# Performance work log

Hardware: AMD Instinct MI355X
Metric: run time of the kernel (lower is better)

The kernel has to match this reference:

```python
import jax, jax.numpy as jnp
import numpy as np

DMODEL = 1024
NHEAD = 16
DHEAD = DMODEL // NHEAD

def _layernorm(x, g, b, eps=1e-5):
    mu = jnp.mean(x, axis=-1, keepdims=True)
    var = jnp.var(x, axis=-1, keepdims=True)
    return (x - mu) * jax.lax.rsqrt(var + eps) * g + b

def setup_inputs() -> dict:
    key = jax.random.key(0)
    ks = jax.random.split(key, 12)
    b, lq, lv, d = 2, 2048, 2048, DMODEL
    s = 1.0 / np.sqrt(d)
    return {
        "q": jax.random.normal(ks[0], (b, lq, d), jnp.float32),
        "k": jax.random.normal(ks[1], (b, lv, d), jnp.float32),
        "v": jax.random.normal(ks[2], (b, lv, d), jnp.float32),
        "qln_g": jnp.ones((d,), jnp.float32),
        "qln_b": jnp.zeros((d,), jnp.float32),
        "kvln_g": jnp.ones((d,), jnp.float32),
        "kvln_b": jnp.zeros((d,), jnp.float32),
        "Wq": jax.random.normal(ks[3], (d, d), jnp.float32) * s,
        "Wk": jax.random.normal(ks[4], (d, d), jnp.float32) * s,
        "Wv": jax.random.normal(ks[5], (d, d), jnp.float32) * s,
        "Wg": jax.random.normal(ks[6], (d, d), jnp.float32) * s,
        "bg": jnp.zeros((d,), jnp.float32),
        "Wo": jax.random.normal(ks[7], (d, d), jnp.float32) * s,
    }

def reference(q, k, v, qln_g, qln_b, kvln_g, kvln_b, Wq, Wk, Wv, Wg, bg, Wo):
    b, lq, d = q.shape
    lv = v.shape[1]
    qn = _layernorm(q, qln_g, qln_b)           # [b, lq, d]
    q_ = qn @ Wq.T
    kk = _layernorm(k, kvln_g, kvln_b) @ Wk.T
    vv = _layernorm(v, kvln_g, kvln_b) @ Wv.T
    qh = q_.reshape(b, lq, NHEAD, DHEAD)       # bqhd
    kh = kk.reshape(b, lv, NHEAD, DHEAD)
    vh = vv.reshape(b, lv, NHEAD, DHEAD)
    scores = jnp.einsum('bqhd,bkhd->bhqk', qh, kh) / np.sqrt(DHEAD)
    attn = jax.nn.softmax(scores, axis=-1)
    y = jnp.einsum('bhqk,bkhd->bqhd', attn, vh).reshape(b, lq, d)
    g = jax.nn.sigmoid(qn @ Wg.T + bg)
    return (y * g) @ Wo.T
```

## Files before the change

### kernel.cpp

```cpp
#include <hip/hip_runtime.h>
#include <hip/hip_bf16.h>

#define DMODEL 1024
#define NHEAD  16
#define DHEAD  64
#define BATCH  2
#define LQ     2048
#define LV     2048
#define ROWS   (BATCH*LQ)
#define WELEMS (DMODEL*DMODEL)
#define BH     (BATCH*NHEAD)

typedef short bf16x8 __attribute__((ext_vector_type(8)));
typedef float f32x4  __attribute__((ext_vector_type(4)));

__device__ __forceinline__ float bf2f(unsigned short s) {
    union { unsigned u; float f; } v; v.u = ((unsigned)s) << 16;
    return v.f;
}
__device__ __forceinline__ unsigned pk_bf(float a, float b) {
    union { __hip_bfloat162 h; unsigned u; } c;
    c.h = __float22bfloat162_rn(make_float2(a, b));
    return c.u;
}

__device__ __forceinline__ void cp16_g2l(const void* g, void* l) {
    __builtin_amdgcn_global_load_lds(
        (const __attribute__((address_space(1))) void*)g,
        (__attribute__((address_space(3))) void*)l,
        16, 0, 0);
}

#define QSCALE (0.125f * 1.4426950408889634f)

__global__ __launch_bounds__(256) void prep_kernel(
    const float* q, const float* k, const float* v,
    const float* qg, const float* qb, const float* kvg, const float* kvb,
    const float* Wq, const float* Wk, const float* Wv, const float* Wg, const float* Wo,
    unsigned short* qn, unsigned short* kn, unsigned short* vn, unsigned short* wb)
{
    __shared__ float rs[4], rq[4];
    int z = blockIdx.y;
    if (z < 5) {
        if (blockIdx.x >= WELEMS / 1024) return;
        const float* srcs[5] = {Wq, Wk, Wv, Wg, Wo};
        const float* s = srcs[z];
        unsigned short* d = wb + (size_t)z * WELEMS;
        int i = (blockIdx.x * 256 + threadIdx.x) * 4;
        float4 x = *(const float4*)(s + i);
        uint2 o = make_uint2(pk_bf(x.x, x.y), pk_bf(x.z, x.w));
        *(uint2*)(d + i) = o;
        return;
    }
    int row = blockIdx.x;
    const float *x, *gp, *bp; unsigned short* o;
    if      (z == 5) { x = q; gp = qg;  bp = qb;  o = qn; }
    else if (z == 6) { x = k; gp = kvg; bp = kvb; o = kn; }
    else             { x = v; gp = kvg; bp = kvb; o = vn; }

    int col = threadIdx.x * 4;
    float4 xv = *(const float4*)(x + (size_t)row * DMODEL + col);
    float s  = xv.x + xv.y + xv.z + xv.w;
    float sq = xv.x*xv.x + xv.y*xv.y + xv.z*xv.z + xv.w*xv.w;
    #pragma unroll
    for (int off = 1; off < 64; off <<= 1) { s += __shfl_xor(s, off); sq += __shfl_xor(sq, off); }

    int wave = threadIdx.x >> 6, lane = threadIdx.x & 63;
    if (lane == 0) { rs[wave] = s; rq[wave] = sq; }
    __syncthreads();
    float ts = rs[0] + rs[1] + rs[2] + rs[3];
    float tq = rq[0] + rq[1] + rq[2] + rq[3];
    float mu  = ts * (1.0f / DMODEL);
    float var = tq * (1.0f / DMODEL) - mu * mu;
    float inv = rsqrtf(var + 1e-5f);

    float4 gv = *(const float4*)(gp + col);
    float4 bv = *(const float4*)(bp + col);
    float r0 = (xv.x - mu) * inv * gv.x + bv.x;
    float r1 = (xv.y - mu) * inv * gv.y + bv.y;
    float r2 = (xv.z - mu) * inv * gv.z + bv.z;
    float r3 = (xv.w - mu) * inv * gv.w + bv.w;
    *(uint2*)(o + (size_t)row * DMODEL + col) = make_uint2(pk_bf(r0, r1), pk_bf(r2, r3));
}

template<int MODE>
__device__ __forceinline__ void gemm256_core(
    const unsigned short* A, const unsigned short* Bw,
    unsigned short* Obf, const float* bias, float scale,
    unsigned short* Al, unsigned short* Bl, int bm, int bn)
{
    int tid  = threadIdx.x;
    int w = tid >> 6, l = tid & 63, quad = l >> 4, L = l & 15;
    int wm = w >> 2, wn = w & 3;

    int c16 = (l & 7) ^ (l >> 3);
    const unsigned short* gAs = A  + (size_t)(bm * 256 + w * 32 + (l >> 3)) * DMODEL + c16 * 8;
    const unsigned short* gBs = Bw + (size_t)(bn * 256 + w * 32 + (l >> 3)) * DMODEL + c16 * 8;
    int dstE = w * 2048;

    #define STG_A(t) do { const unsigned short* s_ = gAs + (t) * 64;          \
        unsigned short* d_ = Al + (((t) & 1) * 16384) + dstE;                 \
        cp16_g2l(s_,              d_);                                        \
        cp16_g2l(s_ +  8 * DMODEL, d_ +  512);                                \
        cp16_g2l(s_ + 16 * DMODEL, d_ + 1024);                                \
        cp16_g2l(s_ + 24 * DMODEL, d_ + 1536); } while (0)
    #define STG_B(t) do { const unsigned short* s_ = gBs + (t) * 64;          \
        unsigned short* d_ = Bl + (((t) & 1) * 16384) + dstE;                 \
        cp16_g2l(s_,              d_);                                        \
        cp16_g2l(s_ +  8 * DMODEL, d_ +  512);                                \
        cp16_g2l(s_ + 16 * DMODEL, d_ + 1024);                                \
        cp16_g2l(s_ + 24 * DMODEL, d_ + 1536); } while (0)

    int sw = (L & 7) << 3;
    int o0 = ( 0 + quad * 8) ^ sw;
    int o1 = (32 + quad * 8) ^ sw;

    f32x4 acc[8][4];
    #pragma unroll
    for (int i = 0; i < 8; ++i)
        #pragma unroll
        for (int j = 0; j < 4; ++j) acc[i][j] = (f32x4){0.f, 0.f, 0.f, 0.f};

    STG_A(0); STG_B(0);

    const int NT = DMODEL / 64;
    for (int g = 0; g < NT; ++g) {
        int s = g & 1;
        if (g + 1 < NT) { STG_A(g + 1); STG_B(g + 1); }
        if (g + 1 < NT) asm volatile("s_waitcnt vmcnt(8)" ::: "memory");
        else            asm volatile("s_waitcnt vmcnt(0)" ::: "memory");
        __builtin_amdgcn_s_barrier();

        const unsigned short* Ab = Al + s * 16384 + (wm * 128) * 64;
        const unsigned short* Bb = Bl + s * 16384 + (wn * 64) * 64;
        bf16x8 bfr[4][2];
        #pragma unroll
        for (int j = 0; j < 4; ++j) {
            bfr[j][0] = *(const bf16x8*)&Bb[(j * 16 + L) * 64 + o0];
            bfr[j][1] = *(const bf16x8*)&Bb[(j * 16 + L) * 64 + o1];
        }
        __builtin_amdgcn_s_setprio(1);
        #pragma unroll
        for (int i2 = 0; i2 < 8; ++i2) {
            bf16x8 a0 = *(const bf16x8*)&Ab[(i2 * 16 + L) * 64 + o0];
            bf16x8 a1 = *(const bf16x8*)&Ab[(i2 * 16 + L) * 64 + o1];
            #pragma unroll
            for (int j = 0; j < 4; ++j) {
                if (MODE == 3) {
                    acc[i2][j] = __builtin_amdgcn_mfma_f32_16x16x32_bf16(a0, bfr[j][0], acc[i2][j], 0, 0, 0);
                    acc[i2][j] = __builtin_amdgcn_mfma_f32_16x16x32_bf16(a1, bfr[j][1], acc[i2][j], 0, 0, 0);
                } else {
                    acc[i2][j] = __builtin_amdgcn_mfma_f32_16x16x32_bf16(bfr[j][0], a0, acc[i2][j], 0, 0, 0);
                    acc[i2][j] = __builtin_amdgcn_mfma_f32_16x16x32_bf16(bfr[j][1], a1, acc[i2][j], 0, 0, 0);
                }
            }
        }
        __builtin_amdgcn_s_setprio(0);
        __builtin_amdgcn_s_barrier();
    }
    #undef STG_A
    #undef STG_B

    #pragma unroll
    for (int i = 0; i < 8; ++i) {
        #pragma unroll
        for (int j = 0; j < 4; ++j) {
            f32x4 a = acc[i][j];
            if (MODE == 3) {
                int gcol  = bn * 256 + wn * 64 + j * 16 + L;
                int grow0 = bm * 256 + wm * 128 + i * 16 + quad * 4;
                int b = grow0 >> 11, key0 = grow0 & 2047;
                int h = gcol >> 6,   dd   = gcol & 63;
                uint2 o = make_uint2(pk_bf(a[0], a[1]), pk_bf(a[2], a[3]));
                *(uint2*)&Obf[(((size_t)(b * NHEAD + h) * DHEAD + dd) << 11) + key0] = o;
            } else {
                int grow  = bm * 256 + wm * 128 + i * 16 + L;
                int gcol0 = bn * 256 + wn * 64 + j * 16 + quad * 4;
                size_t idx = (size_t)grow * DMODEL + gcol0;
                if (MODE == 0) {
                    uint2 o = make_uint2(pk_bf(a[0] * scale, a[1] * scale),
                                         pk_bf(a[2] * scale, a[3] * scale));
                    *(uint2*)&Obf[idx] = o;
                } else {
                    float4 bv = *(const float4*)&bias[gcol0];
                    float s0 = 1.0f / (1.0f + __expf(-(a[0] + bv.x)));
                    float s1 = 1.0f / (1.0f + __expf(-(a[1] + bv.y)));
                    float s2 = 1.0f / (1.0f + __expf(-(a[2] + bv.z)));
                    float s3 = 1.0f / (1.0f + __expf(-(a[3] + bv.w)));
                    *(uint2*)&Obf[idx] = make_uint2(pk_bf(s0, s1), pk_bf(s2, s3));
                }
            }
        }
    }
}

__global__ __launch_bounds__(512, 2) void gemm256_kernel(
    const unsigned short* qn, const unsigned short* kn, const unsigned short* vn,
    const unsigned short* wb,
    unsigned short* qs, unsigned short* kkp, unsigned short* vt, unsigned short* gate,
    const float* bg)
{
    __shared__ __align__(16) unsigned short Al[2 * 256 * 64];
    __shared__ __align__(16) unsigned short Bl[2 * 256 * 64];
    int f = blockIdx.x, xcd = f & 7, s = f >> 3;
    int z  = xcd & 3;
    int bm = ((xcd >> 2) << 3) | (s >> 2);
    int bn = s & 3;
    switch (z) {
        case 0:  gemm256_core<0>(qn, wb + 0 * WELEMS, qs,   nullptr, QSCALE, Al, Bl, bm, bn); break;
        case 1:  gemm256_core<0>(kn, wb + 1 * WELEMS, kkp,  nullptr, 1.0f,   Al, Bl, bm, bn); break;
        case 2:  gemm256_core<3>(vn, wb + 2 * WELEMS, vt,   nullptr, 1.0f,   Al, Bl, bm, bn); break;
        default: gemm256_core<1>(qn, wb + 3 * WELEMS, gate, bg,      1.0f,   Al, Bl, bm, bn); break;
    }
}

template<int MODE>
__device__ __forceinline__ void gemm_bt_core(
    const unsigned short* A, const unsigned short* Bw,
    unsigned short* Obf, float* Of32, const float* bias, float scale,
    unsigned short* Al, unsigned short* Bl, int bm, int bn)
{
    int tid  = threadIdx.x;
    int wave = tid >> 6, lane = tid & 63, quad = lane >> 4, L = lane & 15;
    int wm = wave >> 1, wn = wave & 1;

    int srow = wave * 16 + (lane >> 2);
    int scol = (lane & 3) * 8;
    const unsigned short* gA = A  + (size_t)(bm * 128 + srow) * DMODEL + scol;
    const unsigned short* gB = Bw + (size_t)(bn * 128 + srow) * DMODEL + scol;
    int lofs0 = wave * 16 * 32;
    int lofs1 = (64 + wave * 16) * 32;

    f32x4 acc[4][4];
    #pragma unroll
    for (int i = 0; i < 4; ++i)
        #pragma unroll
        for (int j = 0; j < 4; ++j) acc[i][j] = (f32x4){0.f, 0.f, 0.f, 0.f};

    cp16_g2l(gA,               Al + lofs0);
    cp16_g2l(gA + 64 * DMODEL, Al + lofs1);
    cp16_g2l(gB,               Bl + lofs0);
    cp16_g2l(gB + 64 * DMODEL, Bl + lofs1);

    int buf = 0;
    for (int k0 = 0; k0 < DMODEL; k0 += 32, buf ^= 1) {
        __syncthreads();
        if (k0 + 32 < DMODEL) {
            int nb = (buf ^ 1) * (128 * 32);
            cp16_g2l(gA + k0 + 32,               Al + nb + lofs0);
            cp16_g2l(gA + 64 * DMODEL + k0 + 32, Al + nb + lofs1);
            cp16_g2l(gB + k0 + 32,               Bl + nb + lofs0);
            cp16_g2l(gB + 64 * DMODEL + k0 + 32, Bl + nb + lofs1);
        }
        const unsigned short* Ab = Al + buf * (128 * 32);
        const unsigned short* Bb = Bl + buf * (128 * 32);
        bf16x8 af[4], bfr[4];
        #pragma unroll
        for (int i = 0; i < 4; ++i)
            af[i] = *(const bf16x8*)&Ab[(wm * 64 + i * 16 + L) * 32 + quad * 8];
        #pragma unroll
        for (int j = 0; j < 4; ++j)
            bfr[j] = *(const bf16x8*)&Bb[(wn * 64 + j * 16 + L) * 32 + quad * 8];
        #pragma unroll
        for (int i = 0; i < 4; ++i)
            #pragma unroll
            for (int j = 0; j < 4; ++j) {
                if (MODE == 3)
                    acc[i][j] = __builtin_amdgcn_mfma_f32_16x16x32_bf16(af[i], bfr[j], acc[i][j], 0, 0, 0);
                else
                    acc[i][j] = __builtin_amdgcn_mfma_f32_16x16x32_bf16(bfr[j], af[i], acc[i][j], 0, 0, 0);
            }
    }

    #pragma unroll
    for (int i = 0; i < 4; ++i) {
        #pragma unroll
        for (int j = 0; j < 4; ++j) {
            f32x4 a = acc[i][j];
            int grow  = bm * 128 + wm * 64 + i * 16 + L;
            int gcol0 = bn * 128 + wn * 64 + j * 16 + quad * 4;
            size_t idx = (size_t)grow * DMODEL + gcol0;
            if (MODE == 2) {
                *(f32x4*)&Of32[idx] = a;
            } else if (MODE == 0) {
                uint2 o = make_uint2(pk_bf(a[0] * scale, a[1] * scale),
                                     pk_bf(a[2] * scale, a[3] * scale));
                *(uint2*)&Obf[idx] = o;
            }
        }
    }
}

__device__ __forceinline__ void xcd_map(int& bm, int& bn) {
    int f = blockIdx.y * 8 + blockIdx.x;
    int xcd = f & 7, s = f >> 3;
    bn = s & 7;
    bm = ((s >> 3) << 3) | xcd;
}

__global__ __launch_bounds__(256) void gemm_f32out_kernel(
    const unsigned short* A, const unsigned short* Bw, float* O)
{
    __shared__ __align__(16) unsigned short Al[2 * 128 * 32];
    __shared__ __align__(16) unsigned short Bl[2 * 128 * 32];
    int bm, bn; xcd_map(bm, bn);
    gemm_bt_core<2>(A, Bw, nullptr, O, nullptr, 1.0f, Al, Bl, bm, bn);
}

__global__ __launch_bounds__(256, 4) void attn_kernel(
    const unsigned short* qs, const unsigned short* kk, const unsigned short* vt,
    const unsigned short* gate, unsigned short* yg)
{
    __shared__ __align__(16) unsigned short Kl[2 * 64 * 64];
    __shared__ __align__(16) unsigned short Vl[2 * 64 * 64];

    int tid  = threadIdx.x;
    int wave = tid >> 6, lane = tid & 63, quad = lane >> 4, L = lane & 15;

    int f  = blockIdx.y * 32 + blockIdx.x;
    int bh = (f & 7) * 4 + ((f >> 3) & 3);
    int qt = f >> 5;
    int bb = bh >> 4, h = bh & 15;
    int q0 = qt * 64;

    const unsigned short* Qb =
        qs + ((size_t)(bb * LQ + q0 + wave * 16 + L)) * DMODEL + h * DHEAD;
    bf16x8 aq0 = *(const bf16x8*)(Qb + quad * 8);
    bf16x8 aq1 = *(const bf16x8*)(Qb + 32 + quad * 8);

    f32x4 acc[4];
    #pragma unroll
    for (int nt = 0; nt < 4; ++nt) acc[nt] = (f32x4){0.f, 0.f, 0.f, 0.f};
    f32x4 lacc = (f32x4){0.f, 0.f, 0.f, 0.f};
    bf16x8 ones;
    #pragma unroll
    for (int j = 0; j < 8; ++j) ones[j] = (short)0x3F80;

    int rloc = lane >> 3;
    int c16  = (lane & 7) ^ rloc;
    int key0 = (wave & 1) * 32 + (rloc >> 2) * 8 + (wave >> 1) * 4 + (rloc & 3);

    const unsigned short* gK = kk + (size_t)bb * LV * DMODEL + h * DHEAD
                                  + (size_t)key0 * DMODEL + c16 * 8;
    const unsigned short* gV = vt + ((size_t)((bb * NHEAD + h) * DHEAD
                                  + wave * 16 + rloc)) * LV + c16 * 8;
    char* KlB = (char*)Kl;
    char* VlB = (char*)Vl;
    int dst0 = wave * 2048;

    cp16_g2l(gK,               KlB + dst0);
    cp16_g2l(gK + 16 * DMODEL, KlB + dst0 + 1024);
    cp16_g2l(gV,               VlB + dst0);
    cp16_g2l(gV + 8 * LV,      VlB + dst0 + 1024);

    int sl0 = (quad ^ (L & 7)) * 8;
    int buf = 0;
    for (int it = 0; it < LV / 64; ++it, buf ^= 1) {
        __syncthreads();
        if (it + 1 < LV / 64) {
            gK += 64 * DMODEL; gV += 64;
            int nb = (buf ^ 1) * 8192 + dst0;
            cp16_g2l(gK,               KlB + nb);
            cp16_g2l(gK + 16 * DMODEL, KlB + nb + 1024);
            cp16_g2l(gV,               VlB + nb);
            cp16_g2l(gV + 8 * LV,      VlB + nb + 1024);
        }
        const unsigned short* Kb = Kl + buf * 4096;
        const unsigned short* Vb = Vl + buf * 4096;

        f32x4 zz[4];
        __builtin_amdgcn_s_setprio(1);
        #pragma unroll
        for (int kt = 0; kt < 4; ++kt) {
            bf16x8 bk0 = *(const bf16x8*)&Kb[(kt * 16 + L) * 64 + sl0];
            bf16x8 bk1 = *(const bf16x8*)&Kb[(kt * 16 + L) * 64 + (sl0 ^ 32)];
            f32x4 z = (f32x4){0.f, 0.f, 0.f, 0.f};
            z = __builtin_amdgcn_mfma_f32_16x16x32_bf16(bk0, aq0, z, 0, 0, 0);
            z = __builtin_amdgcn_mfma_f32_16x16x32_bf16(bk1, aq1, z, 0, 0, 0);
            zz[kt] = z;
        }
        __builtin_amdgcn_s_setprio(0);

        union { unsigned u[4]; bf16x8 h; } pa0, pa1;
        pa0.u[0] = pk_bf(__builtin_amdgcn_exp2f(zz[0][0]), __builtin_amdgcn_exp2f(zz[0][1]));
        pa0.u[1] = pk_bf(__builtin_amdgcn_exp2f(zz[0][2]), __builtin_amdgcn_exp2f(zz[0][3]));
        pa0.u[2] = pk_bf(__builtin_amdgcn_exp2f(zz[2][0]), __builtin_amdgcn_exp2f(zz[2][1]));
        pa0.u[3] = pk_bf(__builtin_amdgcn_exp2f(zz[2][2]), __builtin_amdgcn_exp2f(zz[2][3]));
        pa1.u[0] = pk_bf(__builtin_amdgcn_exp2f(zz[1][0]), __builtin_amdgcn_exp2f(zz[1][1]));
        pa1.u[1] = pk_bf(__builtin_amdgcn_exp2f(zz[1][2]), __builtin_amdgcn_exp2f(zz[1][3]));
        pa1.u[2] = pk_bf(__builtin_amdgcn_exp2f(zz[3][0]), __builtin_amdgcn_exp2f(zz[3][1]));
        pa1.u[3] = pk_bf(__builtin_amdgcn_exp2f(zz[3][2]), __builtin_amdgcn_exp2f(zz[3][3]));

        __builtin_amdgcn_s_setprio(1);
        lacc = __builtin_amdgcn_mfma_f32_16x16x32_bf16(ones, pa0.h, lacc, 0, 0, 0);
        lacc = __builtin_amdgcn_mfma_f32_16x16x32_bf16(ones, pa1.h, lacc, 0, 0, 0);
        #pragma unroll
        for (int nt = 0; nt < 4; ++nt) {
            bf16x8 vb0 = *(const bf16x8*)&Vb[(nt * 16 + L) * 64 + sl0];
            bf16x8 vb1 = *(const bf16x8*)&Vb[(nt * 16 + L) * 64 + (sl0 ^ 32)];
            acc[nt] = __builtin_amdgcn_mfma_f32_16x16x32_bf16(vb0, pa0.h, acc[nt], 0, 0, 0);
            acc[nt] = __builtin_amdgcn_mfma_f32_16x16x32_bf16(vb1, pa1.h, acc[nt], 0, 0, 0);
        }
        __builtin_amdgcn_s_setprio(0);
    }

    float inv_l = 1.0f / lacc[0];
    size_t rb = ((size_t)(bb * LQ + q0 + wave * 16 + L)) * DMODEL + h * DHEAD;
    #pragma unroll
    for (int nt = 0; nt < 4; ++nt) {
        size_t idx = rb + nt * 16 + quad * 4;
        ushort4 g = *(const ushort4*)&gate[idx];
        float y0 = acc[nt][0] * inv_l * bf2f(g.x);
        float y1 = acc[nt][1] * inv_l * bf2f(g.y);
        float y2 = acc[nt][2] * inv_l * bf2f(g.z);
        float y3 = acc[nt][3] * inv_l * bf2f(g.w);
        *(uint2*)&yg[idx] = make_uint2(pk_bf(y0, y1), pk_bf(y2, y3));
    }
}

extern "C" void kernel_launch(void* const* d_in, const int* in_sizes, int n_in,
                              void* d_out, int out_size, void* d_ws, size_t ws_size,
                              hipStream_t stream)
{
    const float* q      = (const float*)d_in[0];
    const float* k      = (const float*)d_in[1];
    const float* v      = (const float*)d_in[2];
    const float* qln_g  = (const float*)d_in[3];
    const float* qln_b  = (const float*)d_in[4];
    const float* kvln_g = (const float*)d_in[5];
    const float* kvln_b = (const float*)d_in[6];
    const float* Wq     = (const float*)d_in[7];
    const float* Wk     = (const float*)d_in[8];
    const float* Wv     = (const float*)d_in[9];
    const float* Wg     = (const float*)d_in[10];
    const float* bg     = (const float*)d_in[11];
    const float* Wo     = (const float*)d_in[12];
    float* out = (float*)d_out;

    const size_t T8 = (size_t)ROWS * DMODEL * 2;
    char* ws = (char*)d_ws;
    unsigned short* qn   = (unsigned short*)(ws + 0 * T8);
    unsigned short* kn   = (unsigned short*)(ws + 1 * T8);
    unsigned short* vn   = (unsigned short*)(ws + 2 * T8);
    unsigned short* qs   = (unsigned short*)(ws + 3 * T8);
    unsigned short* kkp  = (unsigned short*)(ws + 4 * T8);
    unsigned short* vt   = (unsigned short*)(ws + 5 * T8);
    unsigned short* gate = (unsigned short*)(ws + 6 * T8);
    unsigned short* yg   = (unsigned short*)(ws + 7 * T8);
    unsigned short* wb   = (unsigned short*)(ws + 8 * T8);

    prep_kernel<<<dim3(ROWS, 8), 256, 0, stream>>>(
        q, k, v, qln_g, qln_b, kvln_g, kvln_b, Wq, Wk, Wv, Wg, Wo, qn, kn, vn, wb);
    gemm256_kernel<<<dim3(256), 512, 0, stream>>>(
        qn, kn, vn, wb, qs, kkp, vt, gate, bg);
    attn_kernel<<<dim3(32, 32), 256, 0, stream>>>(qs, kkp, vt, gate, yg);
    gemm_f32out_kernel<<<dim3(DMODEL / 128, ROWS / 128), 256, 0, stream>>>(yg, wb + 4 * WELEMS, out);
}
```

Before: 236.0 us.

## Restructure GEMM main loop into staged prefetch with interleaved LDS reads and MFMA

The 256x256 GEMM core loop is split into three phases per k-tile, each with its own LDS fragment loads, global-to-LDS copies and MFMA batches. B tiles are staged one iteration ahead in two halves, and A tiles two iterations ahead, with matching vmcnt/lgkmcnt waits and barriers. The staging layout changes to 8-row stripes per wave. The aim is to hide global-load latency and LDS read latency behind matrix-core work. The cost is more barriers per iteration, higher register pressure from holding fragment arrays, and delicate buffer-reuse ordering.

```diff
diff --git a/kernel.cpp b/kernel.cpp
--- a/kernel.cpp
+++ b/kernel.cpp
@@ -94,25 +94,19 @@
     int wm = w >> 2, wn = w & 3;
 
     int c16 = (l & 7) ^ (l >> 3);
-    const unsigned short* gAs = A  + (size_t)(bm * 256 + w * 32 + (l >> 3)) * DMODEL + c16 * 8;
-    const unsigned short* gBs = Bw + (size_t)(bn * 256 + w * 32 + (l >> 3)) * DMODEL + c16 * 8;
-    int dstE = w * 2048;
-
-    #define STG_A(t) do { const unsigned short* s_ = gAs + (t) * 64;          \
-        unsigned short* d_ = Al + (((t) & 1) * 16384) + dstE;                 \
-        cp16_g2l(s_,              d_);                                        \
-        cp16_g2l(s_ +  8 * DMODEL, d_ +  512);                                \
-        cp16_g2l(s_ + 16 * DMODEL, d_ + 1024);                                \
-        cp16_g2l(s_ + 24 * DMODEL, d_ + 1536); } while (0)
-    #define STG_B(t) do { const unsigned short* s_ = gBs + (t) * 64;          \
-        unsigned short* d_ = Bl + (((t) & 1) * 16384) + dstE;                 \
-        cp16_g2l(s_,              d_);                                        \
-        cp16_g2l(s_ +  8 * DMODEL, d_ +  512);                                \
-        cp16_g2l(s_ + 16 * DMODEL, d_ + 1024);                                \
-        cp16_g2l(s_ + 24 * DMODEL, d_ + 1536); } while (0)
+    const unsigned short* gAs = A  + (size_t)(bm * 256 + w * 8 + (l >> 3)) * DMODEL + c16 * 8;
+    const unsigned short* gBs = Bw + (size_t)(bn * 256 + w * 8 + (l >> 3)) * DMODEL + c16 * 8;
+    int dstE = w * 512;
+
+    #define STG_A2(t, ro) do { const unsigned short* s_ = gAs + (size_t)(ro) * DMODEL + (t) * 64; \
+        unsigned short* d_ = Al + ((t) & 1) * 16384 + (ro) * 64 + dstE;                           \
+        cp16_g2l(s_, d_); cp16_g2l(s_ + 64 * DMODEL, d_ + 4096); } while (0)
+    #define STG_B2(t, ro) do { const unsigned short* s_ = gBs + (size_t)(ro) * DMODEL + (t) * 64; \
+        unsigned short* d_ = Bl + ((t) & 1) * 16384 + (ro) * 64 + dstE;                           \
+        cp16_g2l(s_, d_); cp16_g2l(s_ + 64 * DMODEL, d_ + 4096); } while (0)
 
     int sw = (L & 7) << 3;
-    int o0 = ( 0 + quad * 8) ^ sw;
+    int o0 = (quad * 8) ^ sw;
     int o1 = (32 + quad * 8) ^ sw;
 
     f32x4 acc[8][4];
@@ -121,45 +115,92 @@
         #pragma unroll
         for (int j = 0; j < 4; ++j) acc[i][j] = (f32x4){0.f, 0.f, 0.f, 0.f};
 
-    STG_A(0); STG_B(0);
+    STG_A2(0, 0); STG_A2(0, 128); STG_B2(0, 0); STG_B2(0, 128);
+    STG_A2(1, 0); STG_A2(1, 128);
+    asm volatile("s_waitcnt vmcnt(4)" ::: "memory");
+    __builtin_amdgcn_s_barrier();
 
     const int NT = DMODEL / 64;
-    for (int g = 0; g < NT; ++g) {
-        int s = g & 1;
-        if (g + 1 < NT) { STG_A(g + 1); STG_B(g + 1); }
-        if (g + 1 < NT) asm volatile("s_waitcnt vmcnt(8)" ::: "memory");
-        else            asm volatile("s_waitcnt vmcnt(0)" ::: "memory");
-        __builtin_amdgcn_s_barrier();
-
-        const unsigned short* Ab = Al + s * 16384 + (wm * 128) * 64;
-        const unsigned short* Bb = Bl + s * 16384 + (wn * 64) * 64;
-        bf16x8 bfr[4][2];
+    for (int t = 0; t < NT; ++t) {
+        const unsigned short* Ab = Al + (t & 1) * 16384 + wm * 8192;
+        const unsigned short* Bb = Bl + (t & 1) * 16384 + wn * 4096;
+        bf16x8 b0[4], b1[4], a0[2], a1[2], r0v[6], r1v[6];
+
         #pragma unroll
         for (int j = 0; j < 4; ++j) {
-            bfr[j][0] = *(const bf16x8*)&Bb[(j * 16 + L) * 64 + o0];
-            bfr[j][1] = *(const bf16x8*)&Bb[(j * 16 + L) * 64 + o1];
-        }
+            b0[j] = *(const bf16x8*)&Bb[(j * 16 + L) * 64 + o0];
+            b1[j] = *(const bf16x8*)&Bb[(j * 16 + L) * 64 + o1];
+        }
+        #pragma unroll
+        for (int i2 = 0; i2 < 2; ++i2) {
+            a0[i2] = *(const bf16x8*)&Ab[(i2 * 16 + L) * 64 + o0];
+            a1[i2] = *(const bf16x8*)&Ab[(i2 * 16 + L) * 64 + o1];
+        }
+        if (t + 1 < NT) STG_B2(t + 1, 0);
+        __builtin_amdgcn_s_barrier();
         __builtin_amdgcn_s_setprio(1);
         #pragma unroll
-        for (int i2 = 0; i2 < 8; ++i2) {
-            bf16x8 a0 = *(const bf16x8*)&Ab[(i2 * 16 + L) * 64 + o0];
-            bf16x8 a1 = *(const bf16x8*)&Ab[(i2 * 16 + L) * 64 + o1];
+        for (int i2 = 0; i2 < 2; ++i2)
             #pragma unroll
             for (int j = 0; j < 4; ++j) {
                 if (MODE == 3) {
-                    acc[i2][j] = __builtin_amdgcn_mfma_f32_16x16x32_bf16(a0, bfr[j][0], acc[i2][j], 0, 0, 0);
-                    acc[i2][j] = __builtin_amdgcn_mfma_f32_16x16x32_bf16(a1, bfr[j][1], acc[i2][j], 0, 0, 0);
+                    acc[i2][j] = __builtin_amdgcn_mfma_f32_16x16x32_bf16(a0[i2], b0[j], acc[i2][j], 0, 0, 0);
+                    acc[i2][j] = __builtin_amdgcn_mfma_f32_16x16x32_bf16(a1[i2], b1[j], acc[i2][j], 0, 0, 0);
                 } else {
-                    acc[i2][j] = __builtin_amdgcn_mfma_f32_16x16x32_bf16(bfr[j][0], a0, acc[i2][j], 0, 0, 0);
-                    acc[i2][j] = __builtin_amdgcn_mfma_f32_16x16x32_bf16(bfr[j][1], a1, acc[i2][j], 0, 0, 0);
+                    acc[i2][j] = __builtin_amdgcn_mfma_f32_16x16x32_bf16(b0[j], a0[i2], acc[i2][j], 0, 0, 0);
+                    acc[i2][j] = __builtin_amdgcn_mfma_f32_16x16x32_bf16(b1[j], a1[i2], acc[i2][j], 0, 0, 0);
                 }
             }
-        }
         __builtin_amdgcn_s_setprio(0);
         __builtin_amdgcn_s_barrier();
-    }
-    #undef STG_A
-    #undef STG_B
+
+        #pragma unroll
+        for (int r = 0; r < 6; ++r) {
+            r0v[r] = *(const bf16x8*)&Ab[((32 + r * 16) + L) * 64 + o0];
+            r1v[r] = *(const bf16x8*)&Ab[((32 + r * 16) + L) * 64 + o1];
+        }
+        if (t + 1 < NT) STG_B2(t + 1, 128);
+        __builtin_amdgcn_s_barrier();
+        __builtin_amdgcn_s_setprio(1);
+        #pragma unroll
+        for (int i2 = 0; i2 < 2; ++i2)
+            #pragma unroll
+            for (int j = 0; j < 4; ++j) {
+                if (MODE == 3) {
+                    acc[2 + i2][j] = __builtin_amdgcn_mfma_f32_16x16x32_bf16(r0v[i2], b0[j], acc[2 + i2][j], 0, 0, 0);
+                    acc[2 + i2][j] = __builtin_amdgcn_mfma_f32_16x16x32_bf16(r1v[i2], b1[j], acc[2 + i2][j], 0, 0, 0);
+                } else {
+                    acc[2 + i2][j] = __builtin_amdgcn_mfma_f32_16x16x32_bf16(b0[j], r0v[i2], acc[2 + i2][j], 0, 0, 0);
+                    acc[2 + i2][j] = __builtin_amdgcn_mfma_f32_16x16x32_bf16(b1[j], r1v[i2], acc[2 + i2][j], 0, 0, 0);
+                }
+            }
+        __builtin_amdgcn_s_setprio(0);
+        asm volatile("s_waitcnt lgkmcnt(0)" ::: "memory");
+        __builtin_amdgcn_sched_barrier(0);
+        __builtin_amdgcn_s_barrier();
+
+        if (t + 2 < NT) { STG_A2(t + 2, 0); STG_A2(t + 2, 128); }
+        __builtin_amdgcn_s_barrier();
+        __builtin_amdgcn_s_setprio(1);
+        #pragma unroll
+        for (int i2 = 0; i2 < 4; ++i2)
+            #pragma unroll
+            for (int j = 0; j < 4; ++j) {
+                if (MODE == 3) {
+                    acc[4 + i2][j] = __builtin_amdgcn_mfma_f32_16x16x32_bf16(r0v[2 + i2], b0[j], acc[4 + i2][j], 0, 0, 0);
+                    acc[4 + i2][j] = __builtin_amdgcn_mfma_f32_16x16x32_bf16(r1v[2 + i2], b1[j], acc[4 + i2][j], 0, 0, 0);
+                } else {
+                    acc[4 + i2][j] = __builtin_amdgcn_mfma_f32_16x16x32_bf16(b0[j], r0v[2 + i2], acc[4 + i2][j], 0, 0, 0);
+                    acc[4 + i2][j] = __builtin_amdgcn_mfma_f32_16x16x32_bf16(b1[j], r1v[2 + i2], acc[4 + i2][j], 0, 0, 0);
+                }
+            }
+        __builtin_amdgcn_s_setprio(0);
+        if (t + 2 < NT) asm volatile("s_waitcnt vmcnt(4)" ::: "memory");
+        else            asm volatile("s_waitcnt vmcnt(0)" ::: "memory");
+        __builtin_amdgcn_s_barrier();
+    }
+    #undef STG_A2
+    #undef STG_B2
 
     #pragma unroll
     for (int i = 0; i < 8; ++i) {
```

New measurement: 234.2 us. About the same (-0.8%).
